# Kernel optimization log

Hardware: AMD Instinct MI355X
Metric: run time of the kernel (lower is better)

## Reference

```python
import jax, jax.numpy as jnp
import numpy as np

D_MODEL = 1024

def setup_inputs() -> dict:
    key = jax.random.key(0)
    ks = jax.random.split(key, 7)
    x = jax.random.normal(ks[0], (4, 2048, D_MODEL), dtype=jnp.float32)
    s = 1.0 / np.sqrt(D_MODEL)
    Wq = jax.random.uniform(ks[1], (D_MODEL, D_MODEL), jnp.float32, -s, s)
    bq = jax.random.uniform(ks[2], (D_MODEL,), jnp.float32, -s, s)
    Wk = jax.random.uniform(ks[3], (D_MODEL, D_MODEL), jnp.float32, -s, s)
    bk = jax.random.uniform(ks[4], (D_MODEL,), jnp.float32, -s, s)
    Wv = jax.random.uniform(ks[5], (D_MODEL, D_MODEL), jnp.float32, -s, s)
    bv = jax.random.uniform(ks[6], (D_MODEL,), jnp.float32, -s, s)
    return {"x": x, "Wq": Wq, "bq": bq, "Wk": Wk, "bk": bk, "Wv": Wv, "bv": bv}

def reference(x, Wq, bq, Wk, bk, Wv, bv):
    # x: [B, S, D]; Linear weights stored torch-style [out, in] -> y = x @ W.T + b
    B, S, D = x.shape
    q = jnp.einsum('bsd,ed->bse', x, Wq) + bq
    k = jnp.einsum('bsd,ed->bse', x, Wk) + bk
    v = jnp.einsum('bsd,ed->bse', x, Wv) + bv
    scores = jnp.einsum('bqd,bkd->bqk', q, k) / jnp.sqrt(jnp.float32(D))
    causal = jnp.tril(jnp.ones((S, S), dtype=bool))  # True = allowed
    scores = jnp.where(causal[None], scores, -jnp.inf)
    probs = jax.nn.softmax(scores, axis=-1)
    return jnp.einsum('bqk,bkd->bqd', probs, v)
```

## Files before the change

kernel.cpp:

```cpp
#include <hip/hip_runtime.h>
#include <hip/hip_bf16.h>
#include <stdint.h>

using bf16 = __hip_bfloat16;
typedef __bf16 bf16x8 __attribute__((ext_vector_type(8)));
typedef float  f32x4  __attribute__((ext_vector_type(4)));
typedef long   i64;
typedef unsigned char u8;

#define AS1 __attribute__((address_space(1)))
#define AS3 __attribute__((address_space(3)))

__device__ __forceinline__ void async_cp16(const void* g, void* l) {
    __builtin_amdgcn_global_load_lds((const AS1 void*)g, (AS3 void*)l, 16, 0, 0);
}

__device__ __forceinline__ unsigned pk8_lo(float a, float b, unsigned old) {
    return __builtin_amdgcn_cvt_pk_fp8_f32(a, b, old, false);
}

#define SBAR()   do { __builtin_amdgcn_s_barrier(); \
                      __builtin_amdgcn_sched_barrier(0); } while (0)
#define WAITV(N) do { asm volatile("s_waitcnt vmcnt(" #N ")"); \
                      __builtin_amdgcn_sched_barrier(0); } while (0)

__device__ __forceinline__ void ld_bfrag(const char* lB, int wn, int quad, int r16,
                                         bf16x8 (&bfr)[4][2])
{
#pragma unroll
    for (int nt = 0; nt < 4; nt++) {
        int row = wn + nt * 16 + r16;
#pragma unroll
        for (int kk = 0; kk < 2; kk++) {
            int slot = (kk * 4 + quad) ^ (row & 7);
            bfr[nt][kk] = *(const bf16x8*)(lB + row * 128 + slot * 16);
        }
    }
}

__device__ __forceinline__ void ld_afrag(const char* lA, int wm, int quad, int r16, int q,
                                         bf16x8 (&af)[2][2])
{
#pragma unroll
    for (int t = 0; t < 2; t++) {
        int row = wm + (q * 2 + t) * 16 + r16;
#pragma unroll
        for (int kk = 0; kk < 2; kk++) {
            int slot = (kk * 4 + quad) ^ (row & 7);
            af[t][kk] = *(const bf16x8*)(lA + row * 128 + slot * 16);
        }
    }
}

__device__ __forceinline__ void mfma_quad(int q, bf16x8 (&af)[2][2], bf16x8 (&bfr)[4][2],
                                          f32x4 (&acc)[8][4])
{
    __builtin_amdgcn_s_setprio(1);
#pragma unroll
    for (int mt = 0; mt < 2; mt++)
#pragma unroll
        for (int nt = 0; nt < 4; nt++)
#pragma unroll
            for (int kk = 0; kk < 2; kk++)
                acc[q * 2 + mt][nt] = __builtin_amdgcn_mfma_f32_16x16x32_bf16(
                    af[mt][kk], bfr[nt][kk], acc[q * 2 + mt][kk == 0 ? nt : nt], 0, 0, 0);
    __builtin_amdgcn_s_setprio(0);
}

__global__ __launch_bounds__(512, 2) void gemm_qkv(
    const bf16* __restrict__ xb,
    const bf16* __restrict__ Wqb, const bf16* __restrict__ Wkb, const bf16* __restrict__ Wvb,
    const float* __restrict__ bq, const float* __restrict__ bk, const float* __restrict__ bv,
    u8* __restrict__ Qq, u8* __restrict__ Kq, bf16* __restrict__ Vt)
{
    extern __shared__ char smem[];
    const int bn = blockIdx.x, bm = blockIdx.y;
    const int seg = bn >> 2, bn_loc = bn & 3;
    const bf16*  W    = seg == 0 ? Wqb : (seg == 1 ? Wkb : Wvb);
    const float* bias = seg == 0 ? bq  : (seg == 1 ? bk  : bv);

    const int tid  = threadIdx.x;
    const int wave = tid >> 6, lane = tid & 63;
    const int wm = (wave >> 2) * 128, wn = (wave & 3) * 64;
    const int quad = lane >> 4, r16 = lane & 15;

    char* A0 = smem;
    char* A1 = smem + 32768;
    char* B0 = smem + 65536;
    char* B1 = smem + 98304;

    const bf16* Ab = xb + (long)bm * 256 * 1024;
    const bf16* Bb = W  + (long)bn_loc * 256 * 1024;

    const int rl  = lane >> 3;
    const int cbg = (lane & 7) ^ rl;
    const bf16* gA = Ab + (long)(wave * 32 + rl) * 1024 + cbg * 8;
    const bf16* gB = Bb + (long)(wave * 32 + rl) * 1024 + cbg * 8;
    const int woff = wave * 4096;

    auto stage = [&](char* dst, const bf16* src, int k0, int c) {
        async_cp16(src + (long)c * 8192 + k0, dst + woff + c * 1024);
    };

    f32x4 acc[8][4];
    const f32x4 zero = {0.f, 0.f, 0.f, 0.f};
#pragma unroll
    for (int i = 0; i < 8; i++)
#pragma unroll
        for (int j = 0; j < 4; j++) acc[i][j] = zero;

#pragma unroll
    for (int c = 0; c < 4; c++) stage(B0, gB, 0, c);
#pragma unroll
    for (int c = 0; c < 4; c++) stage(A0, gA, 0, c);
#pragma unroll
    for (int c = 0; c < 4; c++) stage(B1, gB, 64, c);
    WAITV(4);
    SBAR();

    bf16x8 bfr[4][2], af[2][2];
#pragma unroll 1
    for (int i = 0; i < 8; ++i) {
        const int kO  = i * 128 + 64;
        const int kE2 = i * 128 + 128;
        const int kO2 = i * 128 + 192;
        const bool pre = (i < 7);

        ld_bfrag(B0, wn, quad, r16, bfr);
        ld_afrag(A0, wm, quad, r16, 0, af);
        stage(A1, gA, kO, 0); stage(A1, gA, kO, 1);
        SBAR();
        mfma_quad(0, af, bfr, acc);
        SBAR();
        ld_afrag(A0, wm, quad, r16, 1, af);
        stage(A1, gA, kO, 2); stage(A1, gA, kO, 3);
        SBAR();
        mfma_quad(1, af, bfr, acc);
        SBAR();
        ld_afrag(A0, wm, quad, r16, 2, af);
        if (pre) { stage(B0, gB, kE2, 0); stage(B0, gB, kE2, 1); }
        SBAR();
        mfma_quad(2, af, bfr, acc);
        SBAR();
        ld_afrag(A0, wm, quad, r16, 3, af);
        if (pre) { stage(B0, gB, kE2, 2); stage(B0, gB, kE2, 3); WAITV(4); }
        else     { WAITV(0); }
        SBAR();
        mfma_quad(3, af, bfr, acc);
        SBAR();
        ld_bfrag(B1, wn, quad, r16, bfr);
        ld_afrag(A1, wm, quad, r16, 0, af);
        if (pre) { stage(A0, gA, kE2, 0); stage(A0, gA, kE2, 1); }
        SBAR();
        mfma_quad(0, af, bfr, acc);
        SBAR();
        ld_afrag(A1, wm, quad, r16, 1, af);
        if (pre) { stage(A0, gA, kE2, 2); stage(A0, gA, kE2, 3); }
        SBAR();
        mfma_quad(1, af, bfr, acc);
        SBAR();
        ld_afrag(A1, wm, quad, r16, 2, af);
        if (pre) { stage(B1, gB, kO2, 0); stage(B1, gB, kO2, 1); }
        SBAR();
        mfma_quad(2, af, bfr, acc);
        SBAR();
        ld_afrag(A1, wm, quad, r16, 3, af);
        if (pre) { stage(B1, gB, kO2, 2); stage(B1, gB, kO2, 3); WAITV(4); }
        SBAR();
        mfma_quad(3, af, bfr, acc);
        SBAR();
    }

    if (seg < 2) {
        u8* O = seg == 0 ? Qq : Kq;
#pragma unroll
        for (int mt = 0; mt < 8; mt++) {
#pragma unroll
            for (int nt = 0; nt < 4; nt++) {
                int col = bn_loc * 256 + wn + nt * 16 + r16;
                float badd = bias[col];
#pragma unroll
                for (int rg = 0; rg < 4; rg++) {
                    long token = (long)bm * 256 + wm + mt * 16 + quad * 4 + rg;
                    float v = acc[mt][nt][rg] + badd;
                    O[token * 1024 + col] = (u8)(pk8_lo(v, v, 0u) & 0xFF);
                }
            }
        }
    } else {
#pragma unroll
        for (int mt = 0; mt < 8; mt++) {
#pragma unroll
            for (int nt = 0; nt < 4; nt++) {
                int col = bn_loc * 256 + wn + nt * 16 + r16;
                float badd = bias[col];
                long token0 = (long)bm * 256 + wm + mt * 16 + quad * 4;
                union { ushort4 u; bf16 h[4]; } o;
#pragma unroll
                for (int rg = 0; rg < 4; rg++)
                    o.h[rg] = __float2bfloat16(acc[mt][nt][rg] + badd);
                *(ushort4*)&Vt[(long)col * 8192 + token0] = o.u;
            }
        }
    }
}

__global__ __launch_bounds__(256, 2) void gemm_scores(
    const u8* __restrict__ Qq, const u8* __restrict__ Kq,
    bf16* __restrict__ P, float* __restrict__ spart)
{
    const int lin = blockIdx.x + 136 * blockIdx.z;
    const int ntg = (lin & 7) * 68 + (lin >> 3);
    const int t = ntg % 136, bz = ntg / 136;
    int bm = (int)((sqrtf(8.f * t + 1.f) - 1.f) * 0.5f);
    while ((bm + 1) * (bm + 2) / 2 <= t) bm++;
    while (bm * (bm + 1) / 2 > t) bm--;
    const int bn = t - bm * (bm + 1) / 2;
    const bool diag = (bn == bm);

    __shared__ u8 sA[2][128 * 128];
    __shared__ u8 sB[2][128 * 128];

    const int tid  = threadIdx.x;
    const int wave = tid >> 6, lane = tid & 63;
    const int wm = (wave >> 1) * 64, wn = (wave & 1) * 64;
    const int quad = lane >> 4, r16 = lane & 15;
    const int whalf = wave & 1;

    const u8* Ab = Qq + (long)bz * 2048 * 1024 + (long)bm * 128 * 1024;
    const u8* Bb = Kq + (long)bz * 2048 * 1024 + (long)bn * 128 * 1024;

    const int rl = lane >> 3;
    const int cb = (lane & 7) ^ rl;
    const u8* gA = Ab + (long)(wave * 32 + rl) * 1024 + cb * 16;
    const u8* gB = Bb + (long)(wave * 32 + rl) * 1024 + cb * 16;

    f32x4 acc[4][4];
    const f32x4 zero = {0.f, 0.f, 0.f, 0.f};
#pragma unroll
    for (int i = 0; i < 4; i++)
#pragma unroll
        for (int j = 0; j < 4; j++) acc[i][j] = zero;

    for (int it = 0; it < 4; ++it) {
        const int k0 = it * 256;
#pragma unroll
        for (int s = 0; s < 2; s++) {
            u8* lA = sA[s] + wave * 32 * 128;
            u8* lB = sB[s] + wave * 32 * 128;
#pragma unroll
            for (int c = 0; c < 4; c++) {
                async_cp16(gA + (long)c * 8 * 1024 + k0 + s * 128, lA + c * 1024);
                async_cp16(gB + (long)c * 8 * 1024 + k0 + s * 128, lB + c * 1024);
            }
        }
        __syncthreads();
#pragma unroll
        for (int s = 0; s < 2; s++) {
#pragma unroll
            for (int kk = 0; kk < 4; kk++) {
                const int g  = kk * 2 + (quad >> 1);
                const int hb = (quad & 1) * 8;
                i64 av[4], bv[4];
#pragma unroll
                for (int t2 = 0; t2 < 4; t2++) {
                    int row  = wm + t2 * 16 + r16;
                    int slot = g ^ (row & 7);
                    av[t2] = *(const i64*)(sA[s] + row * 128 + slot * 16 + hb);
                }
#pragma unroll
                for (int t2 = 0; t2 < 4; t2++) {
                    int row  = wn + t2 * 16 + r16;
                    int slot = g ^ (row & 7);
                    bv[t2] = *(const i64*)(sB[s] + row * 128 + slot * 16 + hb);
                }
#pragma unroll
                for (int mt = 0; mt < 4; mt++)
#pragma unroll
                    for (int nt = 0; nt < 4; nt++)
                        acc[mt][nt] = __builtin_amdgcn_mfma_f32_16x16x32_fp8_fp8(
                            av[mt], bv[nt], acc[mt][nt], 0, 0, 0);
            }
        }
        __syncthreads();
    }

    bf16* Pb = P + (long)bz * 2048 * 2048 + (long)bm * 128 * 2048 + bn * 128;
    float rowsum[4][4];
#pragma unroll
    for (int mt = 0; mt < 4; mt++)
#pragma unroll
        for (int rg = 0; rg < 4; rg++) rowsum[mt][rg] = 0.f;

#pragma unroll
    for (int mt = 0; mt < 4; mt++) {
#pragma unroll
        for (int nt = 0; nt < 4; nt++) {
            int rcol = wn + nt * 16 + r16;
#pragma unroll
            for (int rg = 0; rg < 4; rg++) {
                int rrow = wm + mt * 16 + quad * 4 + rg;
                float e = (diag && rcol > rrow)
                            ? 0.f : __expf(acc[mt][nt][rg] * 0.03125f);
                Pb[(long)rrow * 2048 + rcol] = __float2bfloat16(e);
                rowsum[mt][rg] += e;
            }
        }
    }
#pragma unroll
    for (int off = 1; off < 16; off <<= 1)
#pragma unroll
        for (int mt = 0; mt < 4; mt++)
#pragma unroll
            for (int rg = 0; rg < 4; rg++)
                rowsum[mt][rg] += __shfl_xor(rowsum[mt][rg], off);

    float* red = (float*)sA;
    if (r16 == 0) {
#pragma unroll
        for (int mt = 0; mt < 4; mt++)
#pragma unroll
            for (int rg = 0; rg < 4; rg++)
                red[whalf * 128 + wm + mt * 16 + quad * 4 + rg] = rowsum[mt][rg];
    }
    __syncthreads();
    if (tid < 128)
        spart[((long)bz * 16 + bn) * 2048 + bm * 128 + tid] = red[tid] + red[128 + tid];
}

__global__ __launch_bounds__(256, 2) void gemm_pv(
    const bf16* __restrict__ P, const bf16* __restrict__ Vt,
    const float* __restrict__ spart, float* __restrict__ out)
{
    const int lin = blockIdx.x + 8 * blockIdx.y + 128 * blockIdx.z;
    const int xcd = lin & 7;
    const int m   = lin >> 3;
    const int bn  = m & 7;
    const int g   = xcd + 8 * (m >> 3);
    const int by  = g & 15, bz = g >> 4;
    const int bm  = (bz < 2) ? (15 - by) : by;
    const int nb  = bm + 1;

    __shared__ bf16 sA[2][128 * 64];
    __shared__ bf16 sB[2][128 * 64];
    __shared__ float invl[128];

    const int tid  = threadIdx.x;
    const int wave = tid >> 6, lane = tid & 63;
    const int wm = (wave >> 1) * 64, wn = (wave & 1) * 64;
    const int quad = lane >> 4, r16 = lane & 15;

    if (tid < 128) {
        long base = (long)bz * 16 * 2048 + (long)bm * 128 + tid;
        float l = 0.f;
        for (int j = 0; j < nb; j++) l += spart[base + j * 2048];
        invl[tid] = 1.f / l;
    }

    const bf16* Ab = P  + (long)bz * 2048 * 2048 + (long)bm * 128 * 2048;
    const bf16* Bb = Vt + (long)bz * 2048 + (long)bn * 128 * 8192;

    const int rl = lane >> 3;
    const int cb = (lane & 7) ^ rl;
    const bf16* gA = Ab + (long)(wave * 32 + rl) * 2048 + cb * 8;
    const bf16* gB = Bb + (long)(wave * 32 + rl) * 8192 + cb * 8;

    f32x4 acc[4][4];
    const f32x4 zero = {0.f, 0.f, 0.f, 0.f};
#pragma unroll
    for (int i = 0; i < 4; i++)
#pragma unroll
        for (int j = 0; j < 4; j++) acc[i][j] = zero;

    for (int it = 0; it < nb; ++it) {
        const int k0 = it * 128;
#pragma unroll
        for (int s = 0; s < 2; s++) {
            char* lA = (char*)sA[s] + wave * 32 * 128;
            char* lB = (char*)sB[s] + wave * 32 * 128;
#pragma unroll
            for (int c = 0; c < 4; c++) {
                async_cp16(gA + (long)c * 8 * 2048 + k0 + s * 64, lA + c * 1024);
                async_cp16(gB + (long)c * 8 * 8192 + k0 + s * 64, lB + c * 1024);
            }
        }
        __syncthreads();
#pragma unroll
        for (int s = 0; s < 2; s++) {
#pragma unroll
            for (int kk = 0; kk < 2; kk++) {
                bf16x8 af[4], bfr[4];
#pragma unroll
                for (int t = 0; t < 4; t++) {
                    int row  = wm + t * 16 + r16;
                    int slot = (kk * 4 + quad) ^ (row & 7);
                    af[t] = *(const bf16x8*)((const char*)sA[s] + row * 128 + slot * 16);
                }
#pragma unroll
                for (int t = 0; t < 4; t++) {
                    int row  = wn + t * 16 + r16;
                    int slot = (kk * 4 + quad) ^ (row & 7);
                    bfr[t] = *(const bf16x8*)((const char*)sB[s] + row * 128 + slot * 16);
                }
#pragma unroll
                for (int mt = 0; mt < 4; mt++)
#pragma unroll
                    for (int nt = 0; nt < 4; nt++)
                        acc[mt][nt] = __builtin_amdgcn_mfma_f32_16x16x32_bf16(
                            af[mt], bfr[nt], acc[mt][nt], 0, 0, 0);
            }
        }
        __syncthreads();
    }

    float* Ob = out + (long)bz * 2048 * 1024 + (long)bm * 128 * 1024 + bn * 128;
#pragma unroll
    for (int mt = 0; mt < 4; mt++) {
#pragma unroll
        for (int nt = 0; nt < 4; nt++) {
            int rcol = wn + nt * 16 + r16;
#pragma unroll
            for (int rg = 0; rg < 4; rg++) {
                int rrow = wm + mt * 16 + quad * 4 + rg;
                Ob[(long)rrow * 1024 + rcol] = acc[mt][nt][rg] * invl[rrow];
            }
        }
    }
}

__global__ __launch_bounds__(256) void cvt_all(
    const float* __restrict__ x,
    const float* __restrict__ Wq, const float* __restrict__ Wk, const float* __restrict__ Wv,
    bf16* __restrict__ xb, bf16* __restrict__ dq, bf16* __restrict__ dk, bf16* __restrict__ dv)
{
    int b = blockIdx.x;
    const float* s; bf16* d; long off;
    if (b < 8192) { s = x; d = xb; off = (long)b * 1024; }
    else {
        int w = (b - 8192) >> 10, lb = (b - 8192) & 1023;
        s = w == 0 ? Wq : (w == 1 ? Wk : Wv);
        d = w == 0 ? dq : (w == 1 ? dk : dv);
        off = (long)lb * 1024;
    }
    long i = off + threadIdx.x * 4;
    float4 v = *(const float4*)(s + i);
    union { ushort4 u; bf16 h[4]; } o;
    o.h[0] = __float2bfloat16(v.x);
    o.h[1] = __float2bfloat16(v.y);
    o.h[2] = __float2bfloat16(v.z);
    o.h[3] = __float2bfloat16(v.w);
    *(ushort4*)(d + i) = o.u;
}

extern "C" void kernel_launch(void* const* d_in, const int* in_sizes, int n_in,
                              void* d_out, int out_size, void* d_ws, size_t ws_size,
                              hipStream_t stream)
{
    (void)in_sizes; (void)n_in; (void)out_size; (void)ws_size;
    const float* x  = (const float*)d_in[0];
    const float* Wq = (const float*)d_in[1];
    const float* bq = (const float*)d_in[2];
    const float* Wk = (const float*)d_in[3];
    const float* bk = (const float*)d_in[4];
    const float* Wv = (const float*)d_in[5];
    const float* bv = (const float*)d_in[6];
    float* out = (float*)d_out;

    char* ws = (char*)d_ws;
    bf16* xb  = (bf16*)ws;  ws += (long)8192 * 1024 * 2;
    bf16* Wqb = (bf16*)ws;  ws += (long)1024 * 1024 * 2;
    bf16* Wkb = (bf16*)ws;  ws += (long)1024 * 1024 * 2;
    bf16* Wvb = (bf16*)ws;  ws += (long)1024 * 1024 * 2;
    u8*  Qq   = (u8*)ws;    ws += (long)8192 * 1024;
    u8*  Kq   = (u8*)ws;    ws += (long)8192 * 1024;
    bf16* Vt  = (bf16*)ws;  ws += (long)8192 * 1024 * 2;
    bf16* P   = (bf16*)ws;  ws += (long)4 * 2048 * 2048 * 2;
    float* spart = (float*)ws; ws += (long)4 * 16 * 2048 * 4;

    static bool attr_set = false;
    if (!attr_set) {
        hipFuncSetAttribute(reinterpret_cast<const void*>(gemm_qkv),
                            hipFuncAttributeMaxDynamicSharedMemorySize, 131072);
        attr_set = true;
    }

    cvt_all<<<8192 + 3072, 256, 0, stream>>>(x, Wq, Wk, Wv, xb, Wqb, Wkb, Wvb);

    gemm_qkv<<<dim3(12, 32), 512, 131072, stream>>>(
        xb, Wqb, Wkb, Wvb, bq, bk, bv, Qq, Kq, Vt);

    gemm_scores<<<dim3(136, 1, 4), 256, 0, stream>>>(Qq, Kq, P, spart);

    gemm_pv<<<dim3(8, 16, 4), 256, 0, stream>>>(P, Vt, spart, out);
}
```

Before: 220.2 us.

## Triple-buffer A tiles in QKV GEMM to deepen prefetch

Adds a third LDS buffer for the A (activation) tile and rotates the three buffers, so A loads are issued one K-step further ahead and the vmcnt waits allow more outstanding loads. This is meant to hide global-memory latency in the QKV projection GEMM. LDS use grows from 128 KB to 160 KB per block, which with 512-thread blocks and launch_bounds(512,2) likely drops residency to one block per CU. The extra buffer-index arithmetic in the loop also adds a small cost.

```diff
diff --git a/kernel.cpp b/kernel.cpp
--- a/kernel.cpp
+++ b/kernel.cpp
@@ -63,7 +63,7 @@
 #pragma unroll
             for (int kk = 0; kk < 2; kk++)
                 acc[q * 2 + mt][nt] = __builtin_amdgcn_mfma_f32_16x16x32_bf16(
-                    af[mt][kk], bfr[nt][kk], acc[q * 2 + mt][kk == 0 ? nt : nt], 0, 0, 0);
+                    af[mt][kk], bfr[nt][kk], acc[q * 2 + mt][nt], 0, 0, 0);
     __builtin_amdgcn_s_setprio(0);
 }
 
@@ -84,10 +84,8 @@
     const int wm = (wave >> 2) * 128, wn = (wave & 3) * 64;
     const int quad = lane >> 4, r16 = lane & 15;
 
-    char* A0 = smem;
-    char* A1 = smem + 32768;
-    char* B0 = smem + 65536;
-    char* B1 = smem + 98304;
+    char* B0 = smem + 98304;
+    char* B1 = smem + 131072;
 
     const bf16* Ab = xb + (long)bm * 256 * 1024;
     const bf16* Bb = W  + (long)bn_loc * 256 * 1024;
@@ -110,62 +108,67 @@
         for (int j = 0; j < 4; j++) acc[i][j] = zero;
 
 #pragma unroll
+    for (int c = 0; c < 4; c++) stage(smem, gA, 0, c);
+#pragma unroll
     for (int c = 0; c < 4; c++) stage(B0, gB, 0, c);
 #pragma unroll
-    for (int c = 0; c < 4; c++) stage(A0, gA, 0, c);
+    for (int c = 0; c < 4; c++) stage(smem + 32768, gA, 64, c);
 #pragma unroll
     for (int c = 0; c < 4; c++) stage(B1, gB, 64, c);
-    WAITV(4);
+    WAITV(8);
     SBAR();
 
     bf16x8 bfr[4][2], af[2][2];
 #pragma unroll 1
     for (int i = 0; i < 8; ++i) {
-        const int kO  = i * 128 + 64;
+        char* Ae  = smem + ((2 * i) % 3) * 32768;
+        char* Ao  = smem + ((2 * i + 1) % 3) * 32768;
+        char* An0 = smem + ((2 * i + 2) % 3) * 32768;
+        char* An1 = Ae;
         const int kE2 = i * 128 + 128;
         const int kO2 = i * 128 + 192;
         const bool pre = (i < 7);
 
         ld_bfrag(B0, wn, quad, r16, bfr);
-        ld_afrag(A0, wm, quad, r16, 0, af);
-        stage(A1, gA, kO, 0); stage(A1, gA, kO, 1);
+        ld_afrag(Ae, wm, quad, r16, 0, af);
+        if (pre) { stage(An0, gA, kE2, 0); stage(An0, gA, kE2, 1); }
         SBAR();
         mfma_quad(0, af, bfr, acc);
         SBAR();
-        ld_afrag(A0, wm, quad, r16, 1, af);
-        stage(A1, gA, kO, 2); stage(A1, gA, kO, 3);
+        ld_afrag(Ae, wm, quad, r16, 1, af);
+        if (pre) { stage(An0, gA, kE2, 2); stage(An0, gA, kE2, 3); }
         SBAR();
         mfma_quad(1, af, bfr, acc);
         SBAR();
-        ld_afrag(A0, wm, quad, r16, 2, af);
+        ld_afrag(Ae, wm, quad, r16, 2, af);
         if (pre) { stage(B0, gB, kE2, 0); stage(B0, gB, kE2, 1); }
         SBAR();
         mfma_quad(2, af, bfr, acc);
         SBAR();
-        ld_afrag(A0, wm, quad, r16, 3, af);
-        if (pre) { stage(B0, gB, kE2, 2); stage(B0, gB, kE2, 3); WAITV(4); }
+        ld_afrag(Ae, wm, quad, r16, 3, af);
+        if (pre) { stage(B0, gB, kE2, 2); stage(B0, gB, kE2, 3); WAITV(8); }
         else     { WAITV(0); }
         SBAR();
         mfma_quad(3, af, bfr, acc);
         SBAR();
         ld_bfrag(B1, wn, quad, r16, bfr);
-        ld_afrag(A1, wm, quad, r16, 0, af);
-        if (pre) { stage(A0, gA, kE2, 0); stage(A0, gA, kE2, 1); }
+        ld_afrag(Ao, wm, quad, r16, 0, af);
+        if (pre) { stage(An1, gA, kO2, 0); stage(An1, gA, kO2, 1); }
         SBAR();
         mfma_quad(0, af, bfr, acc);
         SBAR();
-        ld_afrag(A1, wm, quad, r16, 1, af);
-        if (pre) { stage(A0, gA, kE2, 2); stage(A0, gA, kE2, 3); }
+        ld_afrag(Ao, wm, quad, r16, 1, af);
+        if (pre) { stage(An1, gA, kO2, 2); stage(An1, gA, kO2, 3); }
         SBAR();
         mfma_quad(1, af, bfr, acc);
         SBAR();
-        ld_afrag(A1, wm, quad, r16, 2, af);
+        ld_afrag(Ao, wm, quad, r16, 2, af);
         if (pre) { stage(B1, gB, kO2, 0); stage(B1, gB, kO2, 1); }
         SBAR();
         mfma_quad(2, af, bfr, acc);
         SBAR();
-        ld_afrag(A1, wm, quad, r16, 3, af);
-        if (pre) { stage(B1, gB, kO2, 2); stage(B1, gB, kO2, 3); WAITV(4); }
+        ld_afrag(Ao, wm, quad, r16, 3, af);
+        if (pre) { stage(B1, gB, kO2, 2); stage(B1, gB, kO2, 3); WAITV(8); }
         SBAR();
         mfma_quad(3, af, bfr, acc);
         SBAR();
@@ -479,14 +482,14 @@
 
     static bool attr_set = false;
     if (!attr_set) {
-        hipFuncSetAttribute(reinterpret_cast<const void*>(gemm_qkv),
-                            hipFuncAttributeMaxDynamicSharedMemorySize, 131072);
+        (void)hipFuncSetAttribute(reinterpret_cast<const void*>(gemm_qkv),
+                                  hipFuncAttributeMaxDynamicSharedMemorySize, 163840);
         attr_set = true;
     }
 
     cvt_all<<<8192 + 3072, 256, 0, stream>>>(x, Wq, Wk, Wv, xb, Wqb, Wkb, Wvb);
 
-    gemm_qkv<<<dim3(12, 32), 512, 131072, stream>>>(
+    gemm_qkv<<<dim3(12, 32), 512, 163840, stream>>>(
         xb, Wqb, Wkb, Wvb, bq, bk, bv, Qq, Kq, Vt);
 
     gemm_scores<<<dim3(136, 1, 4), 256, 0, stream>>>(Qq, Kq, P, spart);
```

New measurement: 221.0 us. No clear change (+0.4%).
